# Optimization experiments

Hardware: AMD Instinct MI355X
Metric: run time of the kernel (lower is better)

The kernel has to match this reference:

```python
import jax, jax.numpy as jnp
import numpy as np

P = 7      # pool_size
R = 128    # num_rois
KB = 8     # static max bin extent = floor(wh_max / P) = floor(56/7)


def setup_inputs() -> dict:
    key = jax.random.key(0)
    k1, k2, k3 = jax.random.split(key, 3)
    x = jax.random.normal(k1, (1, 256, 64, 64), dtype=jnp.float32)
    xy = jax.random.randint(k2, (R, 2), 0, 8)            # top-left corners
    wh = jax.random.randint(k3, (R, 2), P, 57)           # w,h in [7,56]: every bin non-empty
    rois = jnp.concatenate([xy, wh], axis=1).astype(jnp.int32)  # [R,4] = (x,y,w,h)
    return {"x": x, "rois": rois}


def _bin_indices(coord, size, limit):
    # Replicates: x1 = int(x + ix*rl); x2 = int(x1 + rl); clamp to [0, limit].
    rl = size.astype(jnp.float32) / P                                    # [R]
    starts = jnp.floor(coord[:, None].astype(jnp.float32)
                       + jnp.arange(P, dtype=jnp.float32) * rl[:, None]).astype(jnp.int32)  # [R,P]
    ends = starts + jnp.floor(rl).astype(jnp.int32)[:, None]             # [R,P]
    starts = jnp.maximum(starts, 0)
    ends = jnp.minimum(ends, limit)
    idx = starts[:, :, None] + jnp.arange(KB, dtype=jnp.int32)           # [R,P,KB]
    valid = idx < ends[:, :, None]
    return jnp.clip(idx, 0, limit - 1), valid


def reference(x, rois):
    B, C, H, W = x.shape
    NEG = jnp.finfo(x.dtype).min
    idx_x, val_x = _bin_indices(rois[:, 0], rois[:, 2], W)   # [R,P,KB]
    idx_y, val_y = _bin_indices(rois[:, 1], rois[:, 3], H)   # [R,P,KB]

    def pool_one(iy, vy, ix, vx):
        # iy,ix: [P,KB] row/col indices for this roi's bins; vy,vx: validity masks
        g = jnp.where(vy[None, None, :, :, None], x[:, :, iy, :], NEG).max(axis=3)  # [B,C,P,W]
        g = jnp.where(vx[None, None, None, :, :], g[:, :, :, ix], NEG).max(axis=4)  # [B,C,Py,Px]
        return g

    out = jax.vmap(pool_one)(idx_y, val_y, idx_x, val_x)     # [R,B,C,P,P]
    # torch: view(-1, num_rois, P, P, C).permute(0,1,4,2,3) -> [1, R, C, P, P] (valid for B=1)
    return out.transpose(1, 0, 2, 3, 4)
```

## Files before the change

### kernel.cpp

```cpp
#include <hip/hip_runtime.h>

#define R 128
#define C 256
#define P 7
#define HW 64
#define SW 72

__global__ __launch_bounds__(256) void
roi_pool_kernel(const float* __restrict__ x,
                const int* __restrict__ rois,
                float* __restrict__ out) {
    const int lane = threadIdx.x & 63;
    const int wid  = __builtin_amdgcn_readfirstlane(threadIdx.x >> 6);
    const int gw   = blockIdx.x * 4 + wid;
    const int cp = gw & 127;
    const int r  = gw >> 7;

    __shared__ float vmbuf[4][2 * P * SW];
    float* slab = vmbuf[wid];

    const int rx = rois[r * 4 + 0];
    const int ry = rois[r * 4 + 1];
    const int rw = rois[r * 4 + 2];
    const int rh = rois[r * 4 + 3];

    const float rlx = (float)rw / 7.0f;
    const float rly = (float)rh / 7.0f;
    const int kw = __builtin_amdgcn_readfirstlane((int)rlx);
    const int kh = __builtin_amdgcn_readfirstlane((int)rly);

    const int syv = (int)floorf(__fadd_rn((float)ry, __fmul_rn((float)lane, rly)));
    const int sy0 = __builtin_amdgcn_readlane(syv, 0);
    const int sy1 = __builtin_amdgcn_readlane(syv, 1);
    const int sy2 = __builtin_amdgcn_readlane(syv, 2);
    const int sy3 = __builtin_amdgcn_readlane(syv, 3);
    const int sy4 = __builtin_amdgcn_readlane(syv, 4);
    const int sy5 = __builtin_amdgcn_readlane(syv, 5);
    const int sy6 = __builtin_amdgcn_readlane(syv, 6);

    const float* xc0 = x + ((size_t)cp << 13);
    const float NEG = -3.402823466e38f;
    const bool act = (unsigned)(lane - rx) < (unsigned)rw;

#define BAND(PY, SY, KH)                                                      \
    {                                                                         \
        const float* p = xc0 + (SY) * HW + lane;                              \
        float v0[KH], v1[KH];                                                 \
        _Pragma("unroll")                                                     \
        for (int j = 0; j < KH; ++j) { v0[j] = p[j * HW];                     \
                                       v1[j] = p[j * HW + 4096]; }            \
        float m0 = NEG, m1 = NEG;                                             \
        _Pragma("unroll")                                                     \
        for (int j = 0; j < KH; ++j) {                                        \
            m0 = fmaxf(m0, (j < kh) ? v0[j] : NEG);                           \
            m1 = fmaxf(m1, (j < kh) ? v1[j] : NEG);                           \
        }                                                                     \
        slab[(PY) * SW + lane] = m0;                                          \
        slab[(P + (PY)) * SW + lane] = m1;                                    \
    }

    if (kh <= 4) {
        if (act) {
            BAND(0,sy0,4) BAND(1,sy1,4) BAND(2,sy2,4) BAND(3,sy3,4)
            BAND(4,sy4,4) BAND(5,sy5,4) BAND(6,sy6,4)
        }
    } else {
        if (act) {
            BAND(0,sy0,8) BAND(1,sy1,8) BAND(2,sy2,8) BAND(3,sy3,8)
            BAND(4,sy4,8) BAND(5,sy5,8) BAND(6,sy6,8)
        }
    }
#undef BAND

    if (lane < P * P) {
        const int py = lane / 7;
        const int px = lane - py * 7;
        const int sx = (int)floorf(__fadd_rn((float)rx, __fmul_rn((float)px, rlx)));
        const float* w0 = slab + py * SW + sx;
        const float* w1 = w0 + P * SW;
        float m0, m1;
        if (kw <= 4) {
            float a0 = w0[0], a1 = w0[1], a2 = w0[2], a3 = w0[3];
            float b0 = w1[0], b1 = w1[1], b2 = w1[2], b3 = w1[3];
            m0 = a0; m1 = b0;
            m0 = fmaxf(m0, (1 < kw) ? a1 : NEG); m1 = fmaxf(m1, (1 < kw) ? b1 : NEG);
            m0 = fmaxf(m0, (2 < kw) ? a2 : NEG); m1 = fmaxf(m1, (2 < kw) ? b2 : NEG);
            m0 = fmaxf(m0, (3 < kw) ? a3 : NEG); m1 = fmaxf(m1, (3 < kw) ? b3 : NEG);
        } else {
            float a0 = w0[0], a1 = w0[1], a2 = w0[2], a3 = w0[3];
            float a4 = w0[4], a5 = w0[5], a6 = w0[6], a7 = w0[7];
            float b0 = w1[0], b1 = w1[1], b2 = w1[2], b3 = w1[3];
            float b4 = w1[4], b5 = w1[5], b6 = w1[6], b7 = w1[7];
            m0 = fmaxf(fmaxf(fmaxf(a0, a1), fmaxf(a2, a3)), a4);
            m1 = fmaxf(fmaxf(fmaxf(b0, b1), fmaxf(b2, b3)), b4);
            m0 = fmaxf(m0, (5 < kw) ? a5 : NEG); m1 = fmaxf(m1, (5 < kw) ? b5 : NEG);
            m0 = fmaxf(m0, (6 < kw) ? a6 : NEG); m1 = fmaxf(m1, (6 < kw) ? b6 : NEG);
            m0 = fmaxf(m0, (7 < kw) ? a7 : NEG); m1 = fmaxf(m1, (7 < kw) ? b7 : NEG);
        }
        const size_t base = ((size_t)(r << 8) + (cp << 1)) * (P * P) + lane;
        out[base] = m0;
        out[base + P * P] = m1;
    }
}

extern "C" void kernel_launch(void* const* d_in, const int* in_sizes, int n_in,
                              void* d_out, int out_size, void* d_ws, size_t ws_size,
                              hipStream_t stream) {
    const float* x = (const float*)d_in[0];
    const int* rois = (const int*)d_in[1];
    float* out = (float*)d_out;

    const int grid = (R * C / 2) / 4;
    roi_pool_kernel<<<grid, 256, 0, stream>>>(x, rois, out);
}
```

Measured before the change: 17.67 us.

## Process four channels per wave with float4 row loads into LDS

Each wavefront now handles four channels instead of two. Lanes are split into four 16-lane groups, and each group loads a full 64-wide row of one channel as float4 vectors. The per-lane ROI-column activity mask is dropped, so every lane loads full rows, and the LDS slab is enlarged to hold four channel bands. Half as many waves are launched and each does more vectorized work, which cuts instruction count per byte. The cost is loading columns outside the ROI, larger LDS use, and fewer waves available to hide latency.

```diff
diff --git a/kernel.cpp b/kernel.cpp
--- a/kernel.cpp
+++ b/kernel.cpp
@@ -4,7 +4,8 @@
 #define C 256
 #define P 7
 #define HW 64
-#define SW 72
+#define SROW 68
+#define SLAB (4 * P * SROW + 8)
 
 __global__ __launch_bounds__(256) void
 roi_pool_kernel(const float* __restrict__ x,
@@ -13,10 +14,11 @@
     const int lane = threadIdx.x & 63;
     const int wid  = __builtin_amdgcn_readfirstlane(threadIdx.x >> 6);
     const int gw   = blockIdx.x * 4 + wid;
-    const int cp = gw & 127;
-    const int r  = gw >> 7;
+    const int cq = gw & 63;
+    const int r  = gw >> 6;
+    const int c0 = cq << 2;
 
-    __shared__ float vmbuf[4][2 * P * SW];
+    __shared__ float vmbuf[4][SLAB];
     float* slab = vmbuf[wid];
 
     const int rx = rois[r * 4 + 0];
@@ -38,37 +40,36 @@
     const int sy5 = __builtin_amdgcn_readlane(syv, 5);
     const int sy6 = __builtin_amdgcn_readlane(syv, 6);
 
-    const float* xc0 = x + ((size_t)cp << 13);
+    const int ch = lane >> 4;
+    const int g  = lane & 15;
+    const float* xch = x + ((size_t)(c0 + ch) << 12) + (g << 2);
     const float NEG = -3.402823466e38f;
-    const bool act = (unsigned)(lane - rx) < (unsigned)rw;
+    const float4 NEG4 = make_float4(NEG, NEG, NEG, NEG);
+
+#define MAX4(a, b) make_float4(fmaxf((a).x,(b).x), fmaxf((a).y,(b).y), \
+                               fmaxf((a).z,(b).z), fmaxf((a).w,(b).w))
 
 #define BAND(PY, SY, KH)                                                      \
     {                                                                         \
-        const float* p = xc0 + (SY) * HW + lane;                              \
-        float v0[KH], v1[KH];                                                 \
+        const float4* p = (const float4*)(xch + (SY) * HW);                   \
+        float4 v[KH];                                                         \
         _Pragma("unroll")                                                     \
-        for (int j = 0; j < KH; ++j) { v0[j] = p[j * HW];                     \
-                                       v1[j] = p[j * HW + 4096]; }            \
-        float m0 = NEG, m1 = NEG;                                             \
+        for (int j = 0; j < KH; ++j) v[j] = p[j * 16];                        \
+        float4 m = v[0];                      \
         _Pragma("unroll")                                                     \
-        for (int j = 0; j < KH; ++j) {                                        \
-            m0 = fmaxf(m0, (j < kh) ? v0[j] : NEG);                           \
-            m1 = fmaxf(m1, (j < kh) ? v1[j] : NEG);                           \
+        for (int j = 1; j < KH; ++j) {                                        \
+            float4 t = (j < kh) ? v[j] : NEG4;                                \
+            m = MAX4(m, t);                                                   \
         }                                                                     \
-        slab[(PY) * SW + lane] = m0;                                          \
-        slab[(P + (PY)) * SW + lane] = m1;                                    \
+        *(float4*)(&slab[(ch * P + (PY)) * SROW + (g << 2)]) = m;             \
     }
 
     if (kh <= 4) {
-        if (act) {
-            BAND(0,sy0,4) BAND(1,sy1,4) BAND(2,sy2,4) BAND(3,sy3,4)
-            BAND(4,sy4,4) BAND(5,sy5,4) BAND(6,sy6,4)
-        }
+        BAND(0,sy0,4) BAND(1,sy1,4) BAND(2,sy2,4) BAND(3,sy3,4)
+        BAND(4,sy4,4) BAND(5,sy5,4) BAND(6,sy6,4)
     } else {
-        if (act) {
-            BAND(0,sy0,8) BAND(1,sy1,8) BAND(2,sy2,8) BAND(3,sy3,8)
-            BAND(4,sy4,8) BAND(5,sy5,8) BAND(6,sy6,8)
-        }
+        BAND(0,sy0,8) BAND(1,sy1,8) BAND(2,sy2,8) BAND(3,sy3,8)
+        BAND(4,sy4,8) BAND(5,sy5,8) BAND(6,sy6,8)
     }
 #undef BAND
 
@@ -76,30 +77,29 @@
         const int py = lane / 7;
         const int px = lane - py * 7;
         const int sx = (int)floorf(__fadd_rn((float)rx, __fmul_rn((float)px, rlx)));
-        const float* w0 = slab + py * SW + sx;
-        const float* w1 = w0 + P * SW;
-        float m0, m1;
-        if (kw <= 4) {
-            float a0 = w0[0], a1 = w0[1], a2 = w0[2], a3 = w0[3];
-            float b0 = w1[0], b1 = w1[1], b2 = w1[2], b3 = w1[3];
-            m0 = a0; m1 = b0;
-            m0 = fmaxf(m0, (1 < kw) ? a1 : NEG); m1 = fmaxf(m1, (1 < kw) ? b1 : NEG);
-            m0 = fmaxf(m0, (2 < kw) ? a2 : NEG); m1 = fmaxf(m1, (2 < kw) ? b2 : NEG);
-            m0 = fmaxf(m0, (3 < kw) ? a3 : NEG); m1 = fmaxf(m1, (3 < kw) ? b3 : NEG);
-        } else {
-            float a0 = w0[0], a1 = w0[1], a2 = w0[2], a3 = w0[3];
-            float a4 = w0[4], a5 = w0[5], a6 = w0[6], a7 = w0[7];
-            float b0 = w1[0], b1 = w1[1], b2 = w1[2], b3 = w1[3];
-            float b4 = w1[4], b5 = w1[5], b6 = w1[6], b7 = w1[7];
-            m0 = fmaxf(fmaxf(fmaxf(a0, a1), fmaxf(a2, a3)), a4);
-            m1 = fmaxf(fmaxf(fmaxf(b0, b1), fmaxf(b2, b3)), b4);
-            m0 = fmaxf(m0, (5 < kw) ? a5 : NEG); m1 = fmaxf(m1, (5 < kw) ? b5 : NEG);
-            m0 = fmaxf(m0, (6 < kw) ? a6 : NEG); m1 = fmaxf(m1, (6 < kw) ? b6 : NEG);
-            m0 = fmaxf(m0, (7 < kw) ? a7 : NEG); m1 = fmaxf(m1, (7 < kw) ? b7 : NEG);
+        const float* wp = slab + py * SROW + sx;
+        const size_t obase = ((size_t)(r << 8) + c0) * (P * P) + lane;
+
+        #pragma unroll
+        for (int cc = 0; cc < 4; ++cc) {
+            const float* w = wp + cc * (P * SROW);
+            float m;
+            if (kw <= 4) {
+                float a0 = w[0], a1 = w[1], a2 = w[2], a3 = w[3];
+                m = a0;
+                m = fmaxf(m, (1 < kw) ? a1 : NEG);
+                m = fmaxf(m, (2 < kw) ? a2 : NEG);
+                m = fmaxf(m, (3 < kw) ? a3 : NEG);
+            } else {
+                float a0 = w[0], a1 = w[1], a2 = w[2], a3 = w[3];
+                float a4 = w[4], a5 = w[5], a6 = w[6], a7 = w[7];
+                m = fmaxf(fmaxf(fmaxf(a0, a1), fmaxf(a2, a3)), a4);
+                m = fmaxf(m, (5 < kw) ? a5 : NEG);
+                m = fmaxf(m, (6 < kw) ? a6 : NEG);
+                m = fmaxf(m, (7 < kw) ? a7 : NEG);
+            }
+            out[obase + cc * (P * P)] = m;
         }
-        const size_t base = ((size_t)(r << 8) + (cp << 1)) * (P * P) + lane;
-        out[base] = m0;
-        out[base + P * P] = m1;
     }
 }
 
@@ -110,6 +110,6 @@
     const int* rois = (const int*)d_in[1];
     float* out = (float*)d_out;
 
-    const int grid = (R * C / 2) / 4;
+    const int grid = (R * C / 4) / 4;
     roi_pool_kernel<<<grid, 256, 0, stream>>>(x, rois, out);
 }
```

New measurement: 18.89 us. 6.9% more time.
